# Performance work log

Measured on AMD Instinct MI355X. Metric: run time of the kernel, lower is better.

The kernel has to match this reference:

```python
import jax, jax.numpy as jnp
import numpy as np

NUM_HEADS = 16
ROPE_BASE = 10000.0
NEG_INF = float('-inf')


def _rotate_half_interleaved(x):
    # x: [..., d]; interleaved rotation: (-x2, x1) pairs
    x1 = x[..., ::2]
    x2 = x[..., 1::2]
    return jnp.stack((-x2, x1), axis=-1).reshape(x.shape)


def _rope_tables(seq_len, head_dim, dtype):
    inv_freq = 1.0 / (ROPE_BASE ** (jnp.arange(0, head_dim, 2, dtype=jnp.float32) / head_dim))
    pos = jnp.arange(seq_len, dtype=jnp.float32)
    freqs = pos[:, None] * inv_freq[None, :]          # [S, d/2]
    emb = jnp.concatenate((freqs, freqs), axis=-1)    # [S, d]  (HF-style concat, as in source)
    return jnp.cos(emb).astype(dtype), jnp.sin(emb).astype(dtype)


def setup_inputs() -> dict:
    key = jax.random.key(0)
    ks = jax.random.split(key, 4)
    B, S, H = 2, 2048, 2048
    scale = 0.02
    x = jax.random.normal(ks[0], (B, S, H), dtype=jnp.float32)
    qkv_w = jax.random.normal(ks[1], (3 * H, H), dtype=jnp.float32) * scale
    qkv_b = jnp.zeros((3 * H,), dtype=jnp.float32)
    out_w = jax.random.normal(ks[2], (H, H), dtype=jnp.float32) * scale
    out_b = jnp.zeros((H,), dtype=jnp.float32)
    attention_mask = jnp.ones((B, S), dtype=jnp.int32)
    return {"x": x, "attention_mask": attention_mask, "qkv_w": qkv_w,
            "qkv_b": qkv_b, "out_w": out_w, "out_b": out_b}


def reference(x, attention_mask, qkv_w, qkv_b, out_w, out_b):
    B, S, H = x.shape
    nh = NUM_HEADS
    hd = H // nh
    scale = hd ** -0.5

    qkv = x @ qkv_w.T + qkv_b                            # [B,S,3H]
    qkv = qkv.reshape(B, S, 3, nh, hd).transpose(2, 0, 3, 1, 4)  # [3,B,nh,S,hd]
    q, k, v = qkv[0], qkv[1], qkv[2]

    cos, sin = _rope_tables(S, hd, x.dtype)              # [S,hd]
    cos = cos[None, None, :, :]
    sin = sin[None, None, :, :]
    q = q * cos + _rotate_half_interleaved(q) * sin
    k = k * cos + _rotate_half_interleaved(k) * sin

    scores = jnp.einsum('bhqd,bhkd->bhqk', q, k) * scale  # [B,nh,S,S]
    causal = jnp.triu(jnp.ones((S, S), dtype=bool), k=1)
    scores = jnp.where(causal[None, None], NEG_INF, scores)
    key_mask = (attention_mask == 0)[:, None, None, :]    # [B,1,1,S]
    scores = jnp.where(key_mask, NEG_INF, scores)

    weights = jax.nn.softmax(scores, axis=-1)
    attn = jnp.einsum('bhqk,bhkd->bhqd', weights, v)       # [B,nh,S,hd]
    attn = attn.transpose(0, 2, 1, 3).reshape(B, S, H)
    return attn @ out_w.T + out_b
```

## Files before the change

### kernel.cpp

```cpp
#include <hip/hip_runtime.h>

typedef __bf16 bf16;
typedef __bf16 bf16x2 __attribute__((ext_vector_type(2)));
typedef __bf16 bf16x4 __attribute__((ext_vector_type(4)));
typedef __bf16 bf16x8 __attribute__((ext_vector_type(8)));
typedef float f32x4 __attribute__((ext_vector_type(4)));
typedef float f32x16 __attribute__((ext_vector_type(16)));

#define MFMA_BF16(a, b, c) __builtin_amdgcn_mfma_f32_16x16x32_bf16(a, b, c, 0, 0, 0)
#define MFMA32(a, b, c)    __builtin_amdgcn_mfma_f32_32x32x16_bf16(a, b, c, 0, 0, 0)

__device__ __forceinline__ void async16(const void* g, void* l) {
    __builtin_amdgcn_global_load_lds(
        (const __attribute__((address_space(1))) void*)g,
        (__attribute__((address_space(3))) void*)l,
        16, 0, 0);
}

__device__ __forceinline__ unsigned pack2(float a, float b) {
    bf16x2 t; t[0] = (bf16)a; t[1] = (bf16)b;
    return __builtin_bit_cast(unsigned, t);
}

__device__ __forceinline__ void cvt8_body(const float* __restrict__ in,
                                          bf16* __restrict__ out, int blk) {
    int i = (blk * 256 + (int)threadIdx.x) * 8;
    float4 a = *(const float4*)(in + i);
    float4 b = *(const float4*)(in + i + 4);
    bf16x8 o;
    o[0] = (bf16)a.x; o[1] = (bf16)a.y; o[2] = (bf16)a.z; o[3] = (bf16)a.w;
    o[4] = (bf16)b.x; o[5] = (bf16)b.y; o[6] = (bf16)b.z; o[7] = (bf16)b.w;
    *(bf16x8*)(out + i) = o;
}

__global__ void prep(const float* __restrict__ x, const float* __restrict__ qkvw,
                     const float* __restrict__ outw, const int* __restrict__ am,
                     bf16* __restrict__ xb, bf16* __restrict__ wqkv, bf16* __restrict__ wout,
                     float* __restrict__ cosT, float* __restrict__ sinT,
                     float* __restrict__ mbias) {
    int blk = blockIdx.x;
    if (blk < 4096)        cvt8_body(x,    xb,   blk);
    else if (blk < 10240)  cvt8_body(qkvw, wqkv, blk - 4096);
    else if (blk < 12288)  cvt8_body(outw, wout, blk - 10240);
    else {
        int i = (blk - 12288) * 256 + threadIdx.x;
        int s = i >> 7, d = i & 127, fi = d & 63;
        float inv = exp2f(-(float)fi * (13.287712379549449f / 64.0f));
        float ang = (float)s * inv;
        cosT[i] = cosf(ang);
        sinT[i] = sinf(ang);
        if (i < 2 * 2048) mbias[i] = (am[i] == 0) ? -1.4427e30f : 0.0f;
    }
}

__global__ void __launch_bounds__(512, 2)
qkv256(const bf16* __restrict__ A, const bf16* __restrict__ Bt,
       const float* __restrict__ bias,
       bf16* __restrict__ qb, bf16* __restrict__ kb, bf16* __restrict__ vtb,
       const float* __restrict__ cosT, const float* __restrict__ sinT) {
    constexpr int K = 2048, NT = K >> 5;
    __shared__ __align__(16) bf16 sA[3][8192];
    __shared__ __align__(16) bf16 sB[3][8192];
    const int tid  = threadIdx.x;
    const int lane = tid & 63;
    const int quad = lane >> 4, l15 = lane & 15;
    const int wid  = tid >> 6, wm = wid >> 2, wn = wid & 3;
    const int bm = blockIdx.x, bn = blockIdx.y;

    f32x4 acc[8][4];
#pragma unroll
    for (int i = 0; i < 8; i++)
#pragma unroll
        for (int j = 0; j < 4; j++)
#pragma unroll
            for (int c = 0; c < 4; c++) acc[i][j][c] = 0.0f;

    const int trow = tid >> 3;
    const int u    = (tid & 7) ^ (trow & 7);
    const int hi   = u >> 2, kc = u & 3;
    const bf16* pA0 = A  + (size_t)(bm * 256 +      trow + 128 * hi) * K + kc * 8;
    const bf16* pA1 = A  + (size_t)(bm * 256 + 64 + trow + 128 * hi) * K + kc * 8;
    const bf16* pB0 = Bt + (size_t)(bn * 256 +      trow + 128 * hi) * K + kc * 8;
    const bf16* pB1 = Bt + (size_t)(bn * 256 + 64 + trow + 128 * hi) * K + kc * 8;
    const int ld0 = tid * 8, ld1 = 4096 + tid * 8;

    bf16 *cA = sA[0], *nA = sA[1], *fA = sA[2];
    bf16 *cB = sB[0], *nB = sB[1], *fB = sB[2];

#define STAGE(DA, DB) do {                                   \
        async16(pA0, (DA) + ld0); async16(pA1, (DA) + ld1);  \
        async16(pB0, (DB) + ld0); async16(pB1, (DB) + ld1);  \
        pA0 += 32; pA1 += 32; pB0 += 32; pB1 += 32;          \
    } while (0)

    const int xa = ((quad + 4 * wm) ^ (l15 & 7)) * 8;
    const int xb = ((quad + 4 * (wn >> 1)) ^ (l15 & 7)) * 8;
    const int ra = l15;
    const int rb = (wn & 1) * 64 + l15;

    STAGE(cA, cB);
    STAGE(nA, nB);
    asm volatile("s_waitcnt vmcnt(4)" ::: "memory");
    __builtin_amdgcn_sched_barrier(0);
    __builtin_amdgcn_s_barrier();
    __builtin_amdgcn_sched_barrier(0);

#pragma unroll 1
    for (int t = 0; t < NT; ++t) {
        if (t + 2 < NT) STAGE(fA, fB);
        {
            bf16x8 af[8], bv[4];
#pragma unroll
            for (int mi = 0; mi < 8; mi++)
                af[mi] = *(const bf16x8*)(cA + (mi * 16 + ra) * 64 + xa);
#pragma unroll
            for (int ni = 0; ni < 4; ni++)
                bv[ni] = *(const bf16x8*)(cB + (ni * 16 + rb) * 64 + xb);
#pragma unroll
            for (int mi = 0; mi < 8; mi++)
#pragma unroll
                for (int ni = 0; ni < 4; ni++)
                    acc[mi][ni] = MFMA_BF16(af[mi], bv[ni], acc[mi][ni]);
        }
        __builtin_amdgcn_sched_barrier(0);
        if (t + 1 < NT) {
            if (t + 2 < NT) asm volatile("s_waitcnt vmcnt(4)" ::: "memory");
            else            asm volatile("s_waitcnt vmcnt(0)" ::: "memory");
            __builtin_amdgcn_sched_barrier(0);
            __builtin_amdgcn_s_barrier();
            __builtin_amdgcn_sched_barrier(0);
        }
        bf16* tp;
        tp = cA; cA = nA; nA = fA; fA = tp;
        tp = cB; cB = nB; nB = fB; fB = tp;
    }
#undef STAGE

#pragma unroll
    for (int mi = 0; mi < 8; mi++)
#pragma unroll
        for (int ni = 0; ni < 4; ni++) {
            int col   = bn * 256 + wn * 64 + ni * 16 + l15;
            int which = col >> 11;
            int hcol  = col & 2047;
            int h = hcol >> 7, d = hcol & 127;
            float bv = bias[col];
#pragma unroll
            for (int r = 0; r < 4; r++) {
                int row = bm * 256 + wm * 128 + mi * 16 + quad * 4 + r;
                int b = row >> 11, s = row & 2047;
                float v  = acc[mi][ni][r] + bv;
                float vp = __shfl_xor(v, 1, 64);
                float ov = v;
                if (which < 2) {
                    float c  = cosT[(s << 7) + d];
                    float sn = sinT[(s << 7) + d];
                    ov = v * c + ((d & 1) ? vp : -vp) * sn;
                }
                if (which == 0) ov *= 0.12751743f;
                size_t bh = (size_t)(b * 16 + h);
                if (which == 0)      qb[(bh * 2048 + s) * 128 + d] = (bf16)ov;
                else if (which == 1) kb[(bh * 2048 + s) * 128 + d] = (bf16)ov;
                else                 vtb[(bh * 128 + d) * 2048 + s] = (bf16)ov;
            }
        }
}

template <int EPI>
__global__ void __launch_bounds__(256, 2)
gemm_bt(const bf16* __restrict__ A, const bf16* __restrict__ Bt,
        const float* __restrict__ bias, float* __restrict__ Cf,
        bf16* __restrict__ qb, bf16* __restrict__ kb, bf16* __restrict__ vtb,
        const float* __restrict__ cosT, const float* __restrict__ sinT,
        int M, int N, int K) {
    __shared__ __align__(16) bf16 sA[128 * 64];
    __shared__ __align__(16) bf16 sB[128 * 64];
    const int tid  = threadIdx.x;
    const int lane = tid & 63;
    const int quad = lane >> 4, l15 = lane & 15;
    const int wid = tid >> 6, wm = wid >> 1, wn = wid & 1;
    const int bm = blockIdx.x, bn = blockIdx.y;

    f32x4 acc[4][4];
#pragma unroll
    for (int i = 0; i < 4; i++)
#pragma unroll
        for (int j = 0; j < 4; j++)
#pragma unroll
            for (int c = 0; c < 4; c++) acc[i][j][c] = 0.0f;

    const int r0 = tid >> 3, x0 = tid & 7;
    const int g0 = x0 ^ (r0 & 7);
    const bf16* pa = A  + (size_t)(bm * 128 + r0) * K + g0 * 8;
    const bf16* pb = Bt + (size_t)(bn * 128 + r0) * K + g0 * 8;
    bf16* la = sA + tid * 8;
    bf16* lb = sB + tid * 8;
    const size_t gstep = (size_t)32 * K;

    for (int k0 = 0; k0 < K; k0 += 64) {
#pragma unroll
        for (int i = 0; i < 4; i++) {
            async16(pa + i * gstep, la + i * 2048);
            async16(pb + i * gstep, lb + i * 2048);
        }
        pa += 64; pb += 64;
        __syncthreads();
#pragma unroll
        for (int ks = 0; ks < 2; ks++) {
            bf16x8 af[4], bfr[4];
#pragma unroll
            for (int i = 0; i < 4; i++) {
                int r = wm * 64 + i * 16 + l15;
                int x = (ks * 4 + quad) ^ (r & 7);
                af[i] = *(const bf16x8*)(sA + r * 64 + x * 8);
            }
#pragma unroll
            for (int i = 0; i < 4; i++) {
                int r = wn * 64 + i * 16 + l15;
                int x = (ks * 4 + quad) ^ (r & 7);
                bfr[i] = *(const bf16x8*)(sB + r * 64 + x * 8);
            }
#pragma unroll
            for (int mi = 0; mi < 4; mi++)
#pragma unroll
                for (int ni = 0; ni < 4; ni++)
                    acc[mi][ni] = MFMA_BF16(af[mi], bfr[ni], acc[mi][ni]);
        }
        __syncthreads();
    }

    if (EPI == 0) {
#pragma unroll
        for (int mi = 0; mi < 4; mi++)
#pragma unroll
            for (int ni = 0; ni < 4; ni++) {
                int row0 = bm * 128 + wm * 64 + mi * 16 + quad * 4;
                int col  = bn * 128 + wn * 64 + ni * 16 + l15;
                float bv = bias[col];
#pragma unroll
                for (int r = 0; r < 4; r++)
                    Cf[(size_t)(row0 + r) * N + col] = acc[mi][ni][r] + bv;
            }
    } else {
#pragma unroll
        for (int mi = 0; mi < 4; mi++)
#pragma unroll
            for (int ni = 0; ni < 4; ni++) {
                int col   = bn * 128 + wn * 64 + ni * 16 + l15;
                int which = col >> 11;
                int hcol  = col & 2047;
                int h = hcol >> 7, d = hcol & 127;
                float bv = bias[col];
#pragma unroll
                for (int r = 0; r < 4; r++) {
                    int row = bm * 128 + wm * 64 + mi * 16 + quad * 4 + r;
                    int b = row >> 11, s = row & 2047;
                    float v  = acc[mi][ni][r] + bv;
                    float vp = __shfl_xor(v, 1, 64);
                    float ov = v;
                    if (which < 2) {
                        float c  = cosT[(s << 7) + d];
                        float sn = sinT[(s << 7) + d];
                        ov = v * c + ((d & 1) ? vp : -vp) * sn;
                    }
                    if (which == 0) ov *= 0.12751743f;
                    size_t bh = (size_t)(b * 16 + h);
                    if (which == 0)      qb[(bh * 2048 + s) * 128 + d] = (bf16)ov;
                    else if (which == 1) kb[(bh * 2048 + s) * 128 + d] = (bf16)ov;
                    else                 vtb[(bh * 128 + d) * 2048 + s] = (bf16)ov;
                }
            }
    }
}

__global__ void __launch_bounds__(256, 2)
fattn(const bf16* __restrict__ Q, const bf16* __restrict__ Kg,
      const bf16* __restrict__ Vt, const float* __restrict__ mbias,
      bf16* __restrict__ O, float* __restrict__ Opart, float* __restrict__ mlpart) {
    __shared__ __align__(16) bf16 sK[2][64 * 128];
    __shared__ __align__(16) bf16 sV[2][128 * 64];
    __shared__ __align__(16) float sMB[2048];
    const int tid = threadIdx.x, lane = tid & 63, w = tid >> 6;
    const int l31 = lane & 31, half = lane >> 5;
    const int id = (int)blockIdx.x;
    const int bh = id & 31, v = id >> 5;
    const int p = v >> 1, role = v & 1;
    const int qa = 15 - p;
    const int n1 = role ? (15 - 2 * p) : 17;

    const bf16* Qb  = Q  + (size_t)bh * 2048 * 128;
    const bf16* Kbh = Kg + (size_t)bh * 2048 * 128;
    const bf16* Vbh = Vt + (size_t)bh * 128 * 2048;
    const int b = bh >> 4, hh = bh & 15;
    const float* mbb = mbias + b * 2048;

    const int swk = (l31 & 15) ^ (l31 >> 4);
    const int swv = (l31 & 7) ^ ((l31 >> 3) & 3);
    const int rk = tid >> 4, xk = tid & 15, gkb = xk ^ rk;
    const int rv = tid >> 3, xv = tid & 7;
    const int gv = xv ^ (rv & 7) ^ ((rv >> 3) & 3);

    auto KT = [&](int t) { return role ? (t < n1 ? 17 + t : t - n1) : t; };

    int qt = qa;
    int myq  = qt * 128 + w * 32 + l31;
    int qmin = qt * 128 + w * 32;

    bf16x8 qf[8];
#pragma unroll
    for (int kq = 0; kq < 8; kq++)
        qf[kq] = *(const bf16x8*)(Qb + (size_t)myq * 128 + kq * 16 + half * 8);

    f32x16 oacc[4];
#pragma unroll
    for (int dt = 0; dt < 4; dt++)
#pragma unroll
        for (int c = 0; c < 16; c++) oacc[dt][c] = 0.0f;
    float m_s = -3e38f, l_s = 0.0f;

    {
        float4 t0 = *(const float4*)(mbb + tid * 8);
        float4 t1 = *(const float4*)(mbb + tid * 8 + 4);
        *(float4*)(sMB + tid * 8) = t0;
        *(float4*)(sMB + tid * 8 + 4) = t1;
    }

    {
        int kb0 = KT(0) * 64;
#pragma unroll
        for (int i = 0; i < 4; i++) {
            async16(Kbh + (size_t)(kb0 + rk + i * 16) * 128 + (gkb ^ (i & 1)) * 8,
                    &sK[0][(i * 256 + tid) * 8]);
            async16(Vbh + (size_t)(rv + i * 32) * 2048 + kb0 + gv * 8,
                    &sV[0][(i * 256 + tid) * 8]);
        }
    }
    __syncthreads();

    for (int t = 0; t < 17; t++) {
        if (role && t == n1) {
            float lf = l_s + __shfl_xor(l_s, 32, 64);
            size_t slot = (size_t)(bh * 8 + (qa - 8)) * 2 + 1;
            float* op = Opart + slot * 16384 + (size_t)(w * 32 + l31) * 128;
#pragma unroll
            for (int dt = 0; dt < 4; dt++)
#pragma unroll
                for (int g = 0; g < 4; g++) {
                    float4 o4 = make_float4(oacc[dt][g * 4 + 0], oacc[dt][g * 4 + 1],
                                            oacc[dt][g * 4 + 2], oacc[dt][g * 4 + 3]);
                    *(float4*)(op + dt * 32 + 8 * g + 4 * half) = o4;
                }
            if (half == 0) {
                float* mp = mlpart + (slot * 128 + (w * 32 + l31)) * 2;
                mp[0] = m_s; mp[1] = lf;
            }
#pragma unroll
            for (int dt = 0; dt < 4; dt++)
#pragma unroll
                for (int c = 0; c < 16; c++) oacc[dt][c] = 0.0f;
            m_s = -3e38f; l_s = 0.0f;
            qt = p;
            myq  = qt * 128 + w * 32 + l31;
            qmin = qt * 128 + w * 32;
#pragma unroll
            for (int kq = 0; kq < 8; kq++)
                qf[kq] = *(const bf16x8*)(Qb + (size_t)myq * 128 + kq * 16 + half * 8);
        }

        const int kb0 = KT(t) * 64;
        const int buf = t & 1;
        if (t + 1 < 17) {
            const int nb0 = KT(t + 1) * 64;
#pragma unroll
            for (int i = 0; i < 4; i++) {
                async16(Kbh + (size_t)(nb0 + rk + i * 16) * 128 + (gkb ^ (i & 1)) * 8,
                        &sK[buf ^ 1][(i * 256 + tid) * 8]);
                async16(Vbh + (size_t)(rv + i * 32) * 2048 + nb0 + gv * 8,
                        &sV[buf ^ 1][(i * 256 + tid) * 8]);
            }
        }
        const bf16* sKb = sK[buf];
        const bf16* sVb = sV[buf];

        f32x16 sacc[2];
#pragma unroll
        for (int tt = 0; tt < 2; tt++)
#pragma unroll
            for (int c = 0; c < 16; c++) sacc[tt][c] = 0.0f;
        __builtin_amdgcn_s_setprio(1);
#pragma unroll
        for (int kq = 0; kq < 8; kq++) {
#pragma unroll
            for (int tt = 0; tt < 2; tt++) {
                int row = tt * 32 + l31;
                int x = (kq * 2 + half) ^ swk;
                bf16x8 kf = *(const bf16x8*)(sKb + row * 128 + x * 8);
                sacc[tt] = MFMA32(kf, qf[kq], sacc[tt]);
            }
        }
        __builtin_amdgcn_s_setprio(0);

        float mx = -3e38f;
        if (kb0 + 63 < qmin) {
#pragma unroll
            for (int tt = 0; tt < 2; tt++)
#pragma unroll
                for (int g = 0; g < 4; g++) {
                    float4 mb4 = *(const float4*)(sMB + kb0 + tt * 32 + 8 * g + 4 * half);
#pragma unroll
                    for (int r2 = 0; r2 < 4; r2++) {
                        float vv = sacc[tt][g * 4 + r2] + ((const float*)&mb4)[r2];
                        sacc[tt][g * 4 + r2] = vv;
                        mx = fmaxf(mx, vv);
                    }
                }
        } else {
#pragma unroll
            for (int tt = 0; tt < 2; tt++)
#pragma unroll
                for (int g = 0; g < 4; g++) {
                    float4 mb4 = *(const float4*)(sMB + kb0 + tt * 32 + 8 * g + 4 * half);
#pragma unroll
                    for (int r2 = 0; r2 < 4; r2++) {
                        int sk = kb0 + tt * 32 + 8 * g + 4 * half + r2;
                        float vv = sacc[tt][g * 4 + r2] + ((const float*)&mb4)[r2];
                        vv = (sk > myq) ? -1e30f : vv;
                        sacc[tt][g * 4 + r2] = vv;
                        mx = fmaxf(mx, vv);
                    }
                }
        }

        mx = fmaxf(mx, __shfl_xor(mx, 32, 64));
        float mnew = fmaxf(m_s, mx);
        if (__all(mx - m_s <= 8.0f)) mnew = m_s;
        float alpha = exp2f(m_s - mnew);
        float rs = 0.0f;
#pragma unroll
        for (int tt = 0; tt < 2; tt++)
#pragma unroll
            for (int c = 0; c < 16; c++) {
                float pe = exp2f(sacc[tt][c] - mnew);
                sacc[tt][c] = pe;
                rs += pe;
            }
        l_s = l_s * alpha + rs;
        if (mnew > m_s) {
#pragma unroll
            for (int dt = 0; dt < 4; dt++) oacc[dt] *= alpha;
        }
        m_s = mnew;

#pragma unroll
        for (int tt = 0; tt < 2; tt++) {
            unsigned w8[8];
#pragma unroll
            for (int i = 0; i < 8; i++)
                w8[i] = pack2(sacc[tt][2 * i], sacc[tt][2 * i + 1]);
#pragma unroll
            for (int s2 = 0; s2 < 2; s2++) {
                const int bse = 4 * s2;
                unsigned a0 = half ? w8[bse]     : w8[bse + 2];
                unsigned a1 = half ? w8[bse + 1] : w8[bse + 3];
                unsigned z0 = (unsigned)__shfl_xor((int)a0, 32, 64);
                unsigned z1 = (unsigned)__shfl_xor((int)a1, 32, 64);
                union { unsigned u[4]; bf16x8 vv; } pu;
                pu.u[0] = half ? z0 : w8[bse];
                pu.u[1] = half ? z1 : w8[bse + 1];
                pu.u[2] = half ? w8[bse + 2] : z0;
                pu.u[3] = half ? w8[bse + 3] : z1;
                bf16x8 pf = pu.vv;
                const int c = (tt * 2 + s2) * 2 + half;
                __builtin_amdgcn_s_setprio(1);
#pragma unroll
                for (int dt = 0; dt < 4; dt++) {
                    int row = dt * 32 + l31;
                    int x = c ^ swv;
                    bf16x8 vf = *(const bf16x8*)(sVb + row * 64 + x * 8);
                    oacc[dt] = MFMA32(vf, pf, oacc[dt]);
                }
                __builtin_amdgcn_s_setprio(0);
            }
        }
        __syncthreads();
    }

    float lf = l_s + __shfl_xor(l_s, 32, 64);
    if (role == 0) {
        size_t slot = (size_t)(bh * 8 + (qa - 8)) * 2 + 0;
        float* op = Opart + slot * 16384 + (size_t)(w * 32 + l31) * 128;
#pragma unroll
        for (int dt = 0; dt < 4; dt++)
#pragma unroll
            for (int g = 0; g < 4; g++) {
                float4 o4 = make_float4(oacc[dt][g * 4 + 0], oacc[dt][g * 4 + 1],
                                        oacc[dt][g * 4 + 2], oacc[dt][g * 4 + 3]);
                *(float4*)(op + dt * 32 + 8 * g + 4 * half) = o4;
            }
        if (half == 0) {
            float* mp = mlpart + (slot * 128 + (w * 32 + l31)) * 2;
            mp[0] = m_s; mp[1] = lf;
        }
    } else {
        float inv = 1.0f / lf;
        size_t base = ((size_t)(b * 2048 + myq)) * 2048 + hh * 128;
#pragma unroll
        for (int dt = 0; dt < 4; dt++)
#pragma unroll
            for (int g = 0; g < 4; g++) {
                bf16x4 o4;
#pragma unroll
                for (int r2 = 0; r2 < 4; r2++) o4[r2] = (bf16)(oacc[dt][g * 4 + r2] * inv);
                *(bf16x4*)(O + base + dt * 32 + 8 * g + 4 * half) = o4;
            }
    }
}

__global__ void combine(const float* __restrict__ Opart, const float* __restrict__ mlpart,
                        bf16* __restrict__ attn) {
    int i = blockIdx.x * 256 + threadIdx.x;
    int dq = (i & 31) * 4;
    int row = i >> 5;
    int qloc = row & 127, ba = row >> 7;
    int ai = ba & 7, bh = ba >> 3;
    const float* mlA = mlpart + ((size_t)(ba * 2 + 0) * 128 + qloc) * 2;
    const float* mlB = mlpart + ((size_t)(ba * 2 + 1) * 128 + qloc) * 2;
    float mA = mlA[0], lA = mlA[1], mB = mlB[0], lB = mlB[1];
    float m = fmaxf(mA, mB);
    float wA = exp2f(mA - m), wB = exp2f(mB - m);
    float inv = 1.0f / (wA * lA + wB * lB);
    float4 oA = *(const float4*)(Opart + (size_t)(ba * 2 + 0) * 16384 + qloc * 128 + dq);
    float4 oB = *(const float4*)(Opart + (size_t)(ba * 2 + 1) * 16384 + qloc * 128 + dq);
    int q = (8 + ai) * 128 + qloc;
    int b = bh >> 4, hh = bh & 15;
    bf16x4 o4;
    o4[0] = (bf16)((wA * oA.x + wB * oB.x) * inv);
    o4[1] = (bf16)((wA * oA.y + wB * oB.y) * inv);
    o4[2] = (bf16)((wA * oA.z + wB * oB.z) * inv);
    o4[3] = (bf16)((wA * oA.w + wB * oB.w) * inv);
    *(bf16x4*)(attn + ((size_t)(b * 2048 + q)) * 2048 + hh * 128 + dq) = o4;
}

extern "C" void kernel_launch(void* const* d_in, const int* in_sizes, int n_in,
                              void* d_out, int out_size, void* d_ws, size_t ws_size,
                              hipStream_t stream) {
    const float* x     = (const float*)d_in[0];
    const int*   am    = (const int*)d_in[1];
    const float* qkvw  = (const float*)d_in[2];
    const float* qkvb  = (const float*)d_in[3];
    const float* outw  = (const float*)d_in[4];
    const float* outb  = (const float*)d_in[5];
    float* out = (float*)d_out;

    char* ws = (char*)d_ws;
    bf16*  xb    = (bf16*)(ws);
    bf16*  wqkv  = (bf16*)(ws + (16ull << 20));
    bf16*  wout  = (bf16*)(ws + (40ull << 20));
    bf16*  qb    = (bf16*)(ws + (48ull << 20));
    bf16*  kb    = (bf16*)(ws + (64ull << 20));
    bf16*  vtb   = (bf16*)(ws + (80ull << 20));
    bf16*  attn  = (bf16*)(ws + (96ull << 20));
    float* cosT  = (float*)(ws + (112ull << 20));
    float* sinT  = (float*)(ws + (113ull << 20));
    float* mbias = (float*)(ws + (114ull << 20));
    float* Opart  = (float*)(ws);
    float* mlpart = (float*)(ws + (32ull << 20));

    prep<<<13312, 256, 0, stream>>>(x, qkvw, outw, am, xb, wqkv, wout, cosT, sinT, mbias);

    qkv256<<<dim3(16, 24), 512, 0, stream>>>(
        xb, wqkv, qkvb, qb, kb, vtb, cosT, sinT);

    fattn<<<dim3(512), 256, 0, stream>>>(qb, kb, vtb, mbias, attn, Opart, mlpart);

    combine<<<4096, 256, 0, stream>>>(Opart, mlpart, attn);

    gemm_bt<0><<<dim3(32, 16), 256, 0, stream>>>(
        attn, wout, outb, out, nullptr, nullptr, nullptr, nullptr, nullptr,
        4096, 2048, 2048);
}
```

Before: 463.6 us.

## Deepen QKV GEMM LDS pipeline to four stages with split-phase MFMA scheduling

The QKV projection GEMM goes from a 3-buffer to a 4-buffer LDS ring, so three k-tiles are prefetched ahead. Each iteration is split into two half-tile MFMA phases, with the A and B async loads interleaved between them and s_setprio raised around the MFMA blocks (an 8-wave ping-pong style schedule). The goal is to hide global-load latency and LDS reads behind matrix work. In exchange the kernel needs more LDS (128KB per block) and more barriers per iteration, which may cut occupancy from the requested two blocks per CU.

```diff
diff --git a/kernel.cpp b/kernel.cpp
--- a/kernel.cpp
+++ b/kernel.cpp
@@ -54,13 +54,13 @@
 }
 
 __global__ void __launch_bounds__(512, 2)
-qkv256(const bf16* __restrict__ A, const bf16* __restrict__ Bt,
-       const float* __restrict__ bias,
-       bf16* __restrict__ qb, bf16* __restrict__ kb, bf16* __restrict__ vtb,
-       const float* __restrict__ cosT, const float* __restrict__ sinT) {
+qkv8p(const bf16* __restrict__ A, const bf16* __restrict__ Bt,
+      const float* __restrict__ bias,
+      bf16* __restrict__ qb, bf16* __restrict__ kb, bf16* __restrict__ vtb,
+      const float* __restrict__ cosT, const float* __restrict__ sinT) {
     constexpr int K = 2048, NT = K >> 5;
-    __shared__ __align__(16) bf16 sA[3][8192];
-    __shared__ __align__(16) bf16 sB[3][8192];
+    __shared__ __align__(16) bf16 sA[4][8192];
+    __shared__ __align__(16) bf16 sB[4][8192];
     const int tid  = threadIdx.x;
     const int lane = tid & 63;
     const int quad = lane >> 4, l15 = lane & 15;
@@ -84,57 +84,78 @@
     const bf16* pB1 = Bt + (size_t)(bn * 256 + 64 + trow + 128 * hi) * K + kc * 8;
     const int ld0 = tid * 8, ld1 = 4096 + tid * 8;
 
-    bf16 *cA = sA[0], *nA = sA[1], *fA = sA[2];
-    bf16 *cB = sB[0], *nB = sB[1], *fB = sB[2];
-
-#define STAGE(DA, DB) do {                                   \
-        async16(pA0, (DA) + ld0); async16(pA1, (DA) + ld1);  \
-        async16(pB0, (DB) + ld0); async16(pB1, (DB) + ld1);  \
-        pA0 += 32; pA1 += 32; pB0 += 32; pB1 += 32;          \
-    } while (0)
-
     const int xa = ((quad + 4 * wm) ^ (l15 & 7)) * 8;
     const int xb = ((quad + 4 * (wn >> 1)) ^ (l15 & 7)) * 8;
     const int ra = l15;
     const int rb = (wn & 1) * 64 + l15;
 
-    STAGE(cA, cB);
-    STAGE(nA, nB);
-    asm volatile("s_waitcnt vmcnt(4)" ::: "memory");
+#pragma unroll
+    for (int s = 0; s < 3; ++s) {
+        async16(pA0, &sA[s][0] + ld0); async16(pA1, &sA[s][0] + ld1);
+        pA0 += 32; pA1 += 32;
+        async16(pB0, &sB[s][0] + ld0); async16(pB1, &sB[s][0] + ld1);
+        pB0 += 32; pB1 += 32;
+    }
+    __builtin_amdgcn_sched_barrier(0);
+    asm volatile("s_waitcnt vmcnt(8)" ::: "memory");
     __builtin_amdgcn_sched_barrier(0);
     __builtin_amdgcn_s_barrier();
     __builtin_amdgcn_sched_barrier(0);
 
 #pragma unroll 1
     for (int t = 0; t < NT; ++t) {
-        if (t + 2 < NT) STAGE(fA, fB);
-        {
-            bf16x8 af[8], bv[4];
-#pragma unroll
-            for (int mi = 0; mi < 8; mi++)
-                af[mi] = *(const bf16x8*)(cA + (mi * 16 + ra) * 64 + xa);
+        const bf16* cA = &sA[t & 3][0];
+        const bf16* cB = &sB[t & 3][0];
+        bf16* gA = &sA[(t + 3) & 3][0];
+        bf16* gB = &sB[(t + 3) & 3][0];
+        const bool st = (t + 3 < NT);
+
+        bf16x8 af[4], bv[4];
+#pragma unroll
+        for (int i = 0; i < 4; i++)
+            af[i] = *(const bf16x8*)(cA + ((i * 16 + ra) << 6) + xa);
+#pragma unroll
+        for (int i = 0; i < 4; i++)
+            bv[i] = *(const bf16x8*)(cB + ((i * 16 + rb) << 6) + xb);
+        if (st) { async16(pA0, gA + ld0); async16(pA1, gA + ld1); pA0 += 32; pA1 += 32; }
+        __builtin_amdgcn_sched_barrier(0);
+        __builtin_amdgcn_s_barrier();
+        asm volatile("s_waitcnt lgkmcnt(0)" ::: "memory");
+        __builtin_amdgcn_sched_barrier(0);
+        __builtin_amdgcn_s_setprio(1);
+#pragma unroll
+        for (int mi = 0; mi < 4; mi++)
 #pragma unroll
             for (int ni = 0; ni < 4; ni++)
-                bv[ni] = *(const bf16x8*)(cB + (ni * 16 + rb) * 64 + xb);
-#pragma unroll
-            for (int mi = 0; mi < 8; mi++)
-#pragma unroll
-                for (int ni = 0; ni < 4; ni++)
-                    acc[mi][ni] = MFMA_BF16(af[mi], bv[ni], acc[mi][ni]);
-        }
-        __builtin_amdgcn_sched_barrier(0);
-        if (t + 1 < NT) {
-            if (t + 2 < NT) asm volatile("s_waitcnt vmcnt(4)" ::: "memory");
-            else            asm volatile("s_waitcnt vmcnt(0)" ::: "memory");
-            __builtin_amdgcn_sched_barrier(0);
-            __builtin_amdgcn_s_barrier();
-            __builtin_amdgcn_sched_barrier(0);
-        }
-        bf16* tp;
-        tp = cA; cA = nA; nA = fA; fA = tp;
-        tp = cB; cB = nB; nB = fB; fB = tp;
-    }
-#undef STAGE
+                acc[mi][ni] = MFMA_BF16(af[mi], bv[ni], acc[mi][ni]);
+        __builtin_amdgcn_s_setprio(0);
+        __builtin_amdgcn_sched_barrier(0);
+        __builtin_amdgcn_s_barrier();
+        __builtin_amdgcn_sched_barrier(0);
+
+#pragma unroll
+        for (int i = 0; i < 4; i++)
+            af[i] = *(const bf16x8*)(cA + (((i + 4) * 16 + ra) << 6) + xa);
+        if (st) { async16(pB0, gB + ld0); async16(pB1, gB + ld1); pB0 += 32; pB1 += 32; }
+        __builtin_amdgcn_sched_barrier(0);
+        __builtin_amdgcn_s_barrier();
+        asm volatile("s_waitcnt lgkmcnt(0)" ::: "memory");
+        __builtin_amdgcn_sched_barrier(0);
+        __builtin_amdgcn_s_setprio(1);
+#pragma unroll
+        for (int mi = 0; mi < 4; mi++)
+#pragma unroll
+            for (int ni = 0; ni < 4; ni++)
+                acc[mi + 4][ni] = MFMA_BF16(af[mi], bv[ni], acc[mi + 4][ni]);
+        __builtin_amdgcn_s_setprio(0);
+        __builtin_amdgcn_sched_barrier(0);
+        if (t < NT - 3)       asm volatile("s_waitcnt vmcnt(8)" ::: "memory");
+        else if (t == NT - 3) asm volatile("s_waitcnt vmcnt(4)" ::: "memory");
+        else if (t == NT - 2) asm volatile("s_waitcnt vmcnt(0)" ::: "memory");
+        __builtin_amdgcn_sched_barrier(0);
+        __builtin_amdgcn_s_barrier();
+        __builtin_amdgcn_sched_barrier(0);
+    }
 
 #pragma unroll
     for (int mi = 0; mi < 8; mi++)
@@ -144,12 +165,12 @@
             int which = col >> 11;
             int hcol  = col & 2047;
             int h = hcol >> 7, d = hcol & 127;
-            float bv = bias[col];
+            float bv2 = bias[col];
 #pragma unroll
             for (int r = 0; r < 4; r++) {
                 int row = bm * 256 + wm * 128 + mi * 16 + quad * 4 + r;
                 int b = row >> 11, s = row & 2047;
-                float v  = acc[mi][ni][r] + bv;
+                float v  = acc[mi][ni][r] + bv2;
                 float vp = __shfl_xor(v, 1, 64);
                 float ov = v;
                 if (which < 2) {
@@ -568,7 +589,7 @@
 
     prep<<<13312, 256, 0, stream>>>(x, qkvw, outw, am, xb, wqkv, wout, cosT, sinT, mbias);
 
-    qkv256<<<dim3(16, 24), 512, 0, stream>>>(
+    qkv8p<<<dim3(16, 24), 512, 0, stream>>>(
         xb, wqkv, qkvb, qb, kb, vtb, cosT, sinT);
 
     fattn<<<dim3(512), 256, 0, stream>>>(qb, kb, vtb, mbias, attn, Opart, mlpart);
```

Measured after the change: 426.0 us. 8.1% less time.
